# Kernel optimization log

Hardware: AMD Instinct MI355X
Metric: run time of the kernel (lower is better)

## Reference

```python
import jax, jax.numpy as jnp
import numpy as np

V, D, H, B, S, K = 10000, 128, 512, 32, 512, 2  # vocab, emb, hidden, batch, seq, num_cells

def setup_inputs() -> dict:
    key = jax.random.key(0)
    ks = jax.random.split(key, 8)
    sc_d, sc_h = 1.0 / np.sqrt(D), 1.0 / np.sqrt(H)
    return {
        "x": jax.random.randint(ks[0], (B, S), 0, V),
        "emb_table": jax.random.normal(ks[1], (V, D), jnp.float32),
        "W_ih": jax.random.uniform(ks[2], (K, 4 * H, D), jnp.float32, -sc_d, sc_d),
        "W_hh": jax.random.uniform(ks[3], (K, 4 * H, H), jnp.float32, -sc_h, sc_h),
        "b_ih": jax.random.uniform(ks[4], (K, 4 * H), jnp.float32, -sc_h, sc_h),
        "b_hh": jax.random.uniform(ks[5], (K, 4 * H), jnp.float32, -sc_h, sc_h),
        "W_out": jax.random.uniform(ks[6], (V, H), jnp.float32, -sc_h, sc_h),
        "b_out": jax.random.uniform(ks[7], (V,), jnp.float32, -sc_h, sc_h),
    }

def _mlstm(x_ids_t, emb_t, W_ih, W_hh, b, h0, c0):
    # x_ids_t: (S,B) int, emb_t: (S,B,D). Two LSTMCells; token id parity picks the cell.
    def step(carry, inp):
        h, c = carry                       # (B,H) each
        xt, ids = inp                      # (B,D), (B,)
        gates = (jnp.einsum('bd,kgd->kbg', xt, W_ih)
                 + jnp.einsum('bh,kgh->kbg', h, W_hh)
                 + b[:, None, :])          # (K,B,4H)
        i, f, g, o = jnp.split(gates, 4, axis=-1)
        i, f, o = jax.nn.sigmoid(i), jax.nn.sigmoid(f), jax.nn.sigmoid(o)
        g = jnp.tanh(g)
        c_new = f * c + i * g              # (K,B,H)
        h_new = o * jnp.tanh(c_new)        # (K,B,H)
        sel = (ids % 2)[:, None]           # (B,1) cell index per example
        h_next = jnp.where(sel == 0, h_new[0], h_new[1])
        c_next = jnp.where(sel == 0, c_new[0], c_new[1])
        return (h_next, c_next), h_next
    (_, _), hs = jax.lax.scan(step, (h0, c0), (emb_t, x_ids_t))
    return hs  # (S,B,H)

def reference(x, emb_table, W_ih, W_hh, b_ih, b_hh, W_out, b_out):
    emb = emb_table[x]                     # (B,S,D)
    emb_t = jnp.transpose(emb, (1, 0, 2))  # (S,B,D) time-major
    h0 = jnp.zeros((x.shape[0], W_hh.shape[-1]), emb.dtype)
    hs = _mlstm(x.T, emb_t, W_ih, W_hh, b_ih + b_hh, h0, h0)  # (S,B,H)
    flat = hs.reshape(-1, hs.shape[-1])    # (S*B, H)
    logits = flat @ W_out.T + b_out        # (S*B, V)
    return jax.nn.log_softmax(logits, axis=1)
```

## Files before the change

### kernel.cpp

```cpp
#include <hip/hip_runtime.h>
#include <hip/hip_bf16.h>

typedef __attribute__((ext_vector_type(8))) short short8;
typedef __attribute__((ext_vector_type(4))) float f32x4;
typedef unsigned long long u64;

#define V_N 10000
#define D_E 128
#define H_N 512
#define B_N 32
#define S_N 512

#define SENT64 0xFFFFFFFFFFFFFFFFull

#define OFF_RP    0
#define OFF_EMB   5242880
#define OFF_HS    (OFF_EMB + 4194304)
#define OFF_WOUT  (OFF_HS + 16777216)

__device__ __forceinline__ float ftanh(float x) {
  float e = __expf(-2.f * fabsf(x));
  float r = (1.f - e) / (1.f + e);
  return __builtin_copysignf(r, x);
}

union U128 { f32x4 f; u64 q[2]; };

__global__ void k_prep_emb(const int* __restrict__ x, const float* __restrict__ tab,
                           __hip_bfloat16* __restrict__ emb) {
  int i = blockIdx.x * 256 + threadIdx.x;
  if (i >= S_N * B_N * D_E) return;
  int d  = i & (D_E - 1);
  int sb = i >> 7;
  int b  = sb & (B_N - 1);
  int s  = sb >> 5;
  int tok = x[b * S_N + s];
  emb[i] = __float2bfloat16(tab[tok * D_E + d]);
}

__global__ void k_prep_wout(const float* __restrict__ w, __hip_bfloat16* __restrict__ o) {
  int i = blockIdx.x * 256 + threadIdx.x;
  if (i < V_N * H_N) o[i] = __float2bfloat16(w[i]);
}

__launch_bounds__(512, 1)
__global__ void k_recurrence(const int* __restrict__ x,
                             const float* __restrict__ W_ih, const float* __restrict__ W_hh,
                             const float* __restrict__ b_ih, const float* __restrict__ b_hh,
                             const __hip_bfloat16* __restrict__ emb,
                             __hip_bfloat16* __restrict__ hs)
{
  __shared__ __align__(16) __hip_bfloat16 Bl[32][648];
  __shared__ unsigned short hloc[16][32];

  const int tid = threadIdx.x;
  const int wg  = blockIdx.x;
  const int lane = tid & 63, wv = tid >> 6;
  const int lrow = lane & 15, lk = (lane >> 4) * 8;

  short8 Afrag[20];
  {
    int kcA = lrow >> 3, jpA = (lrow >> 2) & 1, gateA = lrow & 3;
    int grow = kcA * 2048 + gateA * 512 + wg * 16 + wv * 2 + jpA;
    #pragma unroll
    for (int ks = 0; ks < 20; ++ks) {
      int c0 = ks * 32 + lk;
      short8 a;
      #pragma unroll
      for (int e = 0; e < 8; ++e) {
        int c = c0 + e;
        float v = (c < 128) ? W_ih[(size_t)grow * 128 + c]
                            : W_hh[(size_t)grow * 512 + (c - 128)];
        __hip_bfloat16 hb = __float2bfloat16(v);
        a[e] = *(const short*)&hb;
      }
      Afrag[ks] = a;
    }
  }

  const int g  = lane >> 4;
  const int kc = g >> 1, jp = g & 1;
  const int jj = wv * 2 + jp;
  float bias4[4];
  #pragma unroll
  for (int r = 0; r < 4; ++r) {
    int gr = kc * 2048 + r * 512 + wg * 16 + jj;
    bias4[r] = b_ih[gr] + b_hh[gr];
  }

  const int bA = lane & 15, bB = 16 + bA;
  unsigned parA[16], parB[16];
  #pragma unroll
  for (int w = 0; w < 16; ++w) {
    unsigned pa = 0, pb = 0;
    for (int bb = 0; bb < 32; ++bb) {
      pa |= (unsigned)(x[bA * S_N + w * 32 + bb] & 1) << bb;
      pb |= (unsigned)(x[bB * S_N + w * 32 + bb] & 1) << bb;
    }
    parA[w] = pa; parB[w] = pb;
  }

  float csA = 0.f, csB = 0.f;

  for (int t = 0; t < S_N; ++t) {
    {
      const f32x4* e16 = (const f32x4*)(emb + (size_t)t * B_N * D_E);
      int ex = tid >> 4, col = tid & 15;
      *(f32x4*)((char*)&Bl[0][0] + ex * 1296 + col * 16) = e16[tid];
    }
    if (t == 0) {
      for (int i = tid; i < 4096; i += 512) {
        int b = i >> 7, hh = i & 127;
        *(u64*)&Bl[b][128 + hh * 4] = 0ull;
      }
    } else {
      const char* srcb = (const char*)hs + (size_t)(t - 1) * 32768;
      U128 buf[4];
      unsigned pend = 0xFu;
      while (pend) {
        #pragma unroll
        for (int c = 0; c < 4; ++c)
          if (pend & (1u << c))
            asm volatile("global_load_dwordx4 %0, %1, off sc0 sc1"
                         : "=v"(buf[c].f) : "v"(srcb + (c * 8192 + tid * 16)) : "memory");
        asm volatile("s_waitcnt vmcnt(0)" ::: "memory");
        __builtin_amdgcn_sched_barrier(0);
        #pragma unroll
        for (int c = 0; c < 4; ++c)
          if ((pend & (1u << c)) && buf[c].q[0] != SENT64 && buf[c].q[1] != SENT64) {
            int ci = c * 512 + tid;
            *(f32x4*)((char*)&Bl[0][0] + (ci >> 6) * 1296 + 256 + (ci & 63) * 16) = buf[c].f;
            pend &= ~(1u << c);
          }
      }
    }
    __syncthreads();

    f32x4 acc0 = {0.f,0.f,0.f,0.f}, acc1 = {0.f,0.f,0.f,0.f};
    #pragma unroll
    for (int ks = 0; ks < 20; ++ks) {
      int cb = (ks * 32 + lk) * 2;
      short8 b0 = *(const short8*)((const char*)&Bl[0][0] + lrow * 1296 + cb);
      short8 b1 = *(const short8*)((const char*)&Bl[0][0] + (16 + lrow) * 1296 + cb);
      acc0 = __builtin_amdgcn_mfma_f32_16x16x32_bf16(Afrag[ks], b0, acc0, 0, 0, 0);
      acc1 = __builtin_amdgcn_mfma_f32_16x16x32_bf16(Afrag[ks], b1, acc1, 0, 0, 0);
    }

    {
      float iA = 1.f / (1.f + __expf(-(acc0[0] + bias4[0])));
      float fA = 1.f / (1.f + __expf(-(acc0[1] + bias4[1])));
      float gA = ftanh(acc0[2] + bias4[2]);
      float oA = 1.f / (1.f + __expf(-(acc0[3] + bias4[3])));
      float cnA = fA * csA + iA * gA;
      float hnA = oA * ftanh(cnA);

      float iB = 1.f / (1.f + __expf(-(acc1[0] + bias4[0])));
      float fB = 1.f / (1.f + __expf(-(acc1[1] + bias4[1])));
      float gB = ftanh(acc1[2] + bias4[2]);
      float oB = 1.f / (1.f + __expf(-(acc1[3] + bias4[3])));
      float cnB = fB * csB + iB * gB;
      float hnB = oB * ftanh(cnB);

      float pcA = __shfl_xor(cnA, 32), phA = __shfl_xor(hnA, 32);
      float pcB = __shfl_xor(cnB, 32), phB = __shfl_xor(hnB, 32);

      float c0A = kc ? pcA : cnA, c1A = kc ? cnA : pcA;
      float h0A = kc ? phA : hnA, h1A = kc ? hnA : phA;
      float c0B = kc ? pcB : cnB, c1B = kc ? cnB : pcB;
      float h0B = kc ? phB : hnB, h1B = kc ? hnB : phB;

      int selA = (parA[t >> 5] >> (t & 31)) & 1;
      int selB = (parB[t >> 5] >> (t & 31)) & 1;
      csA = selA ? c1A : c0A;  float hA = selA ? h1A : h0A;
      csB = selB ? c1B : c0B;  float hB = selB ? h1B : h0B;

      if (kc == 0) {
        __hip_bfloat16 ha = __float2bfloat16(hA);
        __hip_bfloat16 hb2 = __float2bfloat16(hB);
        hloc[jj][bA] = *(const unsigned short*)&ha;
        hloc[jj][bB] = *(const unsigned short*)&hb2;
      }
    }
    __syncthreads();

    if (tid < 128) {
      int ex = tid >> 2, part = tid & 3;
      u64 v = (u64)hloc[part * 4 + 0][ex]
            | ((u64)hloc[part * 4 + 1][ex] << 16)
            | ((u64)hloc[part * 4 + 2][ex] << 32)
            | ((u64)hloc[part * 4 + 3][ex] << 48);
      u64* dst = (u64*)hs + (size_t)t * 4096 + ex * 128 + wg * 4 + part;
      __hip_atomic_store(dst, v, __ATOMIC_RELAXED, __HIP_MEMORY_SCOPE_AGENT);
    }
  }
}

__launch_bounds__(256, 2)
__global__ void k_gemm(const __hip_bfloat16* __restrict__ hs,
                       const __hip_bfloat16* __restrict__ wout,
                       const float* __restrict__ b_out,
                       float* __restrict__ out,
                       float* __restrict__ rowpart)
{
  __shared__ __hip_bfloat16 Al[128][72];
  __shared__ __hip_bfloat16 Wt[128][72];
  __shared__ float sumLDS[2][128];
  const int tid = threadIdx.x;
  const int tn = blockIdx.x, tm = blockIdx.y;
  const int lane = tid & 63, wv = tid >> 6;
  const int mq = wv & 1, nq = wv >> 1;
  const int lrow = lane & 15, lk = (lane >> 4) * 8;
  f32x4 acc[4][4] = {};

  const int ar = tid >> 3, ac = (tid & 7) * 8;
  for (int k0 = 0; k0 < 512; k0 += 64) {
    __syncthreads();
    #pragma unroll
    for (int rr = 0; rr < 4; ++rr) {
      int r = ar + rr * 32;
      short8 av = *(const short8*)(hs + ((size_t)(tm * 128 + r)) * 512 + k0 + ac);
      *(short8*)&Al[r][ac] = av;
      int v = tn * 128 + r;
      short8 wvv = {};
      if (v < V_N) wvv = *(const short8*)(wout + (size_t)v * 512 + k0 + ac);
      *(short8*)&Wt[r][ac] = wvv;
    }
    __syncthreads();
    #pragma unroll
    for (int ks = 0; ks < 2; ++ks) {
      int kb = ks * 32 + lk;
      short8 af[4], bf[4];
      #pragma unroll
      for (int i = 0; i < 4; ++i) af[i] = *(const short8*)&Al[mq * 64 + i * 16 + lrow][kb];
      #pragma unroll
      for (int i = 0; i < 4; ++i) bf[i] = *(const short8*)&Wt[nq * 64 + i * 16 + lrow][kb];
      #pragma unroll
      for (int i = 0; i < 4; ++i)
        #pragma unroll
        for (int jx = 0; jx < 4; ++jx)
          acc[i][jx] = __builtin_amdgcn_mfma_f32_16x16x32_bf16(af[i], bf[jx], acc[i][jx], 0, 0, 0);
    }
  }
  const int rbase = tm * 128 + mq * 64 + (lane >> 4) * 4;
  const int cbase = tn * 128 + nq * 64 + (lane & 15);
  float esum[4][4];
  #pragma unroll
  for (int i = 0; i < 4; ++i)
    #pragma unroll
    for (int r = 0; r < 4; ++r) esum[i][r] = 0.f;

  #pragma unroll
  for (int i = 0; i < 4; ++i) {
    #pragma unroll
    for (int jx = 0; jx < 4; ++jx) {
      int col = cbase + jx * 16;
      if (col < V_N) {
        float bo = b_out[col];
        #pragma unroll
        for (int r = 0; r < 4; ++r) {
          int row = rbase + i * 16 + r;
          float lg = acc[i][jx][r] + bo;
          __hip_bfloat16* lrow16 =
            (__hip_bfloat16*)((char*)out + (size_t)row * (V_N * 4) + V_N * 2);
          lrow16[col] = __float2bfloat16(lg);
          esum[i][r] += __expf(lg);
        }
      }
    }
  }
  #pragma unroll
  for (int i = 0; i < 4; ++i) {
    #pragma unroll
    for (int r = 0; r < 4; ++r) {
      float s = esum[i][r];
      s += __shfl_xor(s, 1); s += __shfl_xor(s, 2);
      s += __shfl_xor(s, 4); s += __shfl_xor(s, 8);
      if ((lane & 15) == 0)
        sumLDS[nq][mq * 64 + i * 16 + (lane >> 4) * 4 + r] = s;
    }
  }
  __syncthreads();
  if (tid < 128)
    rowpart[(size_t)(tm * 128 + tid) * 80 + tn] = sumLDS[0][tid] + sumLDS[1][tid];
}

__launch_bounds__(256)
__global__ void k_lsm_fix(float* __restrict__ out, const float* __restrict__ rowpart) {
  const int r = blockIdx.x;
  const int tid = threadIdx.x;
  const float* rp = rowpart + (size_t)r * 80;
  float s = 0.f;
  for (int p = 0; p < 79; ++p) s += rp[p];
  float lse = __logf(s);

  const f32x4* src = (const f32x4*)((const char*)out + (size_t)r * (V_N * 4) + V_N * 2);
  U128 c[5];
  #pragma unroll
  for (int i = 0; i < 5; ++i) {
    int idx = tid + i * 256;
    if (idx < 1250) c[i].f = src[idx];
  }
  __syncthreads();
  float* dst = out + (size_t)r * V_N;
  #pragma unroll
  for (int i = 0; i < 5; ++i) {
    int idx = tid + i * 256;
    if (idx < 1250) {
      const unsigned short* u = (const unsigned short*)&c[i];
      float4 lo, hi;
      lo.x = __uint_as_float((unsigned)u[0] << 16) - lse;
      lo.y = __uint_as_float((unsigned)u[1] << 16) - lse;
      lo.z = __uint_as_float((unsigned)u[2] << 16) - lse;
      lo.w = __uint_as_float((unsigned)u[3] << 16) - lse;
      hi.x = __uint_as_float((unsigned)u[4] << 16) - lse;
      hi.y = __uint_as_float((unsigned)u[5] << 16) - lse;
      hi.z = __uint_as_float((unsigned)u[6] << 16) - lse;
      hi.w = __uint_as_float((unsigned)u[7] << 16) - lse;
      *(float4*)(dst + idx * 8)     = lo;
      *(float4*)(dst + idx * 8 + 4) = hi;
    }
  }
}

extern "C" void kernel_launch(void* const* d_in, const int* in_sizes, int n_in,
                              void* d_out, int out_size, void* d_ws, size_t ws_size,
                              hipStream_t stream) {
  const int*   x    = (const int*)d_in[0];
  const float* tab  = (const float*)d_in[1];
  const float* Wih  = (const float*)d_in[2];
  const float* Whh  = (const float*)d_in[3];
  const float* bih  = (const float*)d_in[4];
  const float* bhh  = (const float*)d_in[5];
  const float* Wout = (const float*)d_in[6];
  const float* bout = (const float*)d_in[7];
  float* out = (float*)d_out;

  char* ws = (char*)d_ws;
  float*           rowpart = (float*)(ws + OFF_RP);
  __hip_bfloat16*  emb     = (__hip_bfloat16*)(ws + OFF_EMB);
  __hip_bfloat16*  hsbuf   = (__hip_bfloat16*)(ws + OFF_HS);
  __hip_bfloat16*  wob     = (__hip_bfloat16*)(ws + OFF_WOUT);

  hipMemsetAsync(hsbuf, 0xFF, (size_t)S_N * B_N * H_N * 2, stream);
  k_prep_emb<<<(S_N * B_N * D_E) / 256, 256, 0, stream>>>(x, tab, emb);
  k_prep_wout<<<(V_N * H_N) / 256, 256, 0, stream>>>(Wout, wob);
  k_recurrence<<<32, 512, 0, stream>>>(x, Wih, Whh, bih, bhh, emb, hsbuf);
  k_gemm<<<dim3(79, 128), 256, 0, stream>>>(hsbuf, wob, bout, out, rowpart);
  k_lsm_fix<<<16384, 256, 0, stream>>>(out, rowpart);
}
```

Baseline: 2.288 ms.

## Publish hidden state via direct shuffled stores and use LDS-direct swizzled GEMM loads

Measured after the change: 2.279 ms. Within noise of the previous version (-0.4%).

```diff
diff --git a/kernel.cpp b/kernel.cpp
--- a/kernel.cpp
+++ b/kernel.cpp
@@ -6,25 +6,30 @@
 typedef unsigned long long u64;
 
 #define V_N 10000
+#define V_PAD 10112
 #define D_E 128
 #define H_N 512
 #define B_N 32
 #define S_N 512
 
 #define SENT64 0xFFFFFFFFFFFFFFFFull
+#define SENT32 0xFFFFFFFFu
 
 #define OFF_RP    0
 #define OFF_EMB   5242880
 #define OFF_HS    (OFF_EMB + 4194304)
 #define OFF_WOUT  (OFF_HS + 16777216)
 
+typedef __attribute__((address_space(1))) const unsigned gas_u32;
+typedef __attribute__((address_space(3))) unsigned las_u32;
+
 __device__ __forceinline__ float ftanh(float x) {
   float e = __expf(-2.f * fabsf(x));
   float r = (1.f - e) / (1.f + e);
   return __builtin_copysignf(r, x);
 }
 
-union U128 { f32x4 f; u64 q[2]; };
+union U128 { f32x4 f; u64 q[2]; unsigned w[4]; };
 
 __global__ void k_prep_emb(const int* __restrict__ x, const float* __restrict__ tab,
                            __hip_bfloat16* __restrict__ emb) {
@@ -40,7 +45,8 @@
 
 __global__ void k_prep_wout(const float* __restrict__ w, __hip_bfloat16* __restrict__ o) {
   int i = blockIdx.x * 256 + threadIdx.x;
-  if (i < V_N * H_N) o[i] = __float2bfloat16(w[i]);
+  if (i >= V_PAD * H_N) return;
+  o[i] = (i < V_N * H_N) ? __float2bfloat16(w[i]) : __float2bfloat16(0.f);
 }
 
 __launch_bounds__(512, 1)
@@ -51,7 +57,6 @@
                              __hip_bfloat16* __restrict__ hs)
 {
   __shared__ __align__(16) __hip_bfloat16 Bl[32][648];
-  __shared__ unsigned short hloc[16][32];
 
   const int tid = threadIdx.x;
   const int wg  = blockIdx.x;
@@ -127,7 +132,9 @@
         __builtin_amdgcn_sched_barrier(0);
         #pragma unroll
         for (int c = 0; c < 4; ++c)
-          if ((pend & (1u << c)) && buf[c].q[0] != SENT64 && buf[c].q[1] != SENT64) {
+          if ((pend & (1u << c)) &&
+              buf[c].w[0] != SENT32 && buf[c].w[1] != SENT32 &&
+              buf[c].w[2] != SENT32 && buf[c].w[3] != SENT32) {
             int ci = c * 512 + tid;
             *(f32x4*)((char*)&Bl[0][0] + (ci >> 6) * 1296 + 256 + (ci & 63) * 16) = buf[c].f;
             pend &= ~(1u << c);
@@ -174,24 +181,23 @@
       csA = selA ? c1A : c0A;  float hA = selA ? h1A : h0A;
       csB = selB ? c1B : c0B;  float hB = selB ? h1B : h0B;
 
-      if (kc == 0) {
-        __hip_bfloat16 ha = __float2bfloat16(hA);
-        __hip_bfloat16 hb2 = __float2bfloat16(hB);
-        hloc[jj][bA] = *(const unsigned short*)&ha;
-        hloc[jj][bB] = *(const unsigned short*)&hb2;
+      __hip_bfloat16 ha = __float2bfloat16(hA);
+      __hip_bfloat16 hb2 = __float2bfloat16(hB);
+      unsigned hA16 = *(const unsigned short*)&ha;
+      unsigned hB16 = *(const unsigned short*)&hb2;
+      unsigned qA = (unsigned)__shfl_xor((int)hA16, 16);
+      unsigned qB = (unsigned)__shfl_xor((int)hB16, 16);
+      if (lane < 16) {
+        unsigned* h32 = (unsigned*)hs + (size_t)t * 8192;
+        unsigned vA = hA16 | (qA << 16);
+        unsigned vB = hB16 | (qB << 16);
+        __hip_atomic_store(h32 + lane * 256 + wg * 8 + wv, vA,
+                           __ATOMIC_RELAXED, __HIP_MEMORY_SCOPE_AGENT);
+        __hip_atomic_store(h32 + (lane + 16) * 256 + wg * 8 + wv, vB,
+                           __ATOMIC_RELAXED, __HIP_MEMORY_SCOPE_AGENT);
       }
     }
     __syncthreads();
-
-    if (tid < 128) {
-      int ex = tid >> 2, part = tid & 3;
-      u64 v = (u64)hloc[part * 4 + 0][ex]
-            | ((u64)hloc[part * 4 + 1][ex] << 16)
-            | ((u64)hloc[part * 4 + 2][ex] << 32)
-            | ((u64)hloc[part * 4 + 3][ex] << 48);
-      u64* dst = (u64*)hs + (size_t)t * 4096 + ex * 128 + wg * 4 + part;
-      __hip_atomic_store(dst, v, __ATOMIC_RELAXED, __HIP_MEMORY_SCOPE_AGENT);
-    }
   }
 }
 
@@ -202,38 +208,46 @@
                        float* __restrict__ out,
                        float* __restrict__ rowpart)
 {
-  __shared__ __hip_bfloat16 Al[128][72];
-  __shared__ __hip_bfloat16 Wt[128][72];
+  __shared__ __align__(16) char AlB[16384];
+  __shared__ __align__(16) char WtB[16384];
   __shared__ float sumLDS[2][128];
   const int tid = threadIdx.x;
   const int tn = blockIdx.x, tm = blockIdx.y;
   const int lane = tid & 63, wv = tid >> 6;
   const int mq = wv & 1, nq = wv >> 1;
-  const int lrow = lane & 15, lk = (lane >> 4) * 8;
+  const int lrow = lane & 15;
+  const int swz = lrow & 7;
   f32x4 acc[4][4] = {};
 
-  const int ar = tid >> 3, ac = (tid & 7) * 8;
+  const int ci0 = wv * 64 + lane;
   for (int k0 = 0; k0 < 512; k0 += 64) {
     __syncthreads();
     #pragma unroll
-    for (int rr = 0; rr < 4; ++rr) {
-      int r = ar + rr * 32;
-      short8 av = *(const short8*)(hs + ((size_t)(tm * 128 + r)) * 512 + k0 + ac);
-      *(short8*)&Al[r][ac] = av;
-      int v = tn * 128 + r;
-      short8 wvv = {};
-      if (v < V_N) wvv = *(const short8*)(wout + (size_t)v * 512 + k0 + ac);
-      *(short8*)&Wt[r][ac] = wvv;
-    }
+    for (int g2 = 0; g2 < 4; ++g2) {
+      int ci = g2 * 256 + ci0;
+      int row = ci >> 3, pos = ci & 7;
+      int lc  = pos ^ (row & 7);
+      const __hip_bfloat16* ga = hs + ((size_t)(tm * 128 + row)) * 512 + k0 + lc * 8;
+      __builtin_amdgcn_global_load_lds((gas_u32*)ga,
+          (las_u32*)(AlB + ci * 16), 16, 0, 0);
+      const __hip_bfloat16* gw = wout + ((size_t)(tn * 128 + row)) * 512 + k0 + lc * 8;
+      __builtin_amdgcn_global_load_lds((gas_u32*)gw,
+          (las_u32*)(WtB + ci * 16), 16, 0, 0);
+    }
+    asm volatile("s_waitcnt vmcnt(0)" ::: "memory");
     __syncthreads();
+
     #pragma unroll
     for (int ks = 0; ks < 2; ++ks) {
-      int kb = ks * 32 + lk;
+      int q = ks * 4 + (lane >> 4);
+      int p16 = (q ^ swz) << 4;
       short8 af[4], bf[4];
       #pragma unroll
-      for (int i = 0; i < 4; ++i) af[i] = *(const short8*)&Al[mq * 64 + i * 16 + lrow][kb];
+      for (int i = 0; i < 4; ++i)
+        af[i] = *(const short8*)(AlB + (mq * 64 + i * 16 + lrow) * 128 + p16);
       #pragma unroll
-      for (int i = 0; i < 4; ++i) bf[i] = *(const short8*)&Wt[nq * 64 + i * 16 + lrow][kb];
+      for (int i = 0; i < 4; ++i)
+        bf[i] = *(const short8*)(WtB + (nq * 64 + i * 16 + lrow) * 128 + p16);
       #pragma unroll
       for (int i = 0; i < 4; ++i)
         #pragma unroll
@@ -343,7 +357,7 @@
 
   hipMemsetAsync(hsbuf, 0xFF, (size_t)S_N * B_N * H_N * 2, stream);
   k_prep_emb<<<(S_N * B_N * D_E) / 256, 256, 0, stream>>>(x, tab, emb);
-  k_prep_wout<<<(V_N * H_N) / 256, 256, 0, stream>>>(Wout, wob);
+  k_prep_wout<<<(V_PAD * H_N) / 256, 256, 0, stream>>>(Wout, wob);
   k_recurrence<<<32, 512, 0, stream>>>(x, Wih, Whh, bih, bhh, emb, hsbuf);
   k_gemm<<<dim3(79, 128), 256, 0, stream>>>(hsbuf, wob, bout, out, rowpart);
   k_lsm_fix<<<16384, 256, 0, stream>>>(out, rowpart);
```
